# Kernel tuning notes

Hardware: AMD Instinct MI355X
Metric: run time of the kernel (lower is better)

The kernel has to match this reference:

```python
import jax, jax.numpy as jnp
import numpy as np


def _div_tree_level(n_agents, level):
    # Deterministic reproduction of get_division_tree (seeded shuffle), row `level`.
    rng = np.random.RandomState(0)
    perm = rng.permutation(n_agents)
    max_div = int(np.ceil(np.log2(n_agents)))
    levels = np.zeros((max_div + 1, n_agents), dtype=np.int64)
    for ith in range(1, max_div + 1):
        levels[ith] = levels[ith - 1]
        for j in range(n_agents):
            seg = j // (n_agents / 2 ** ith)
            if int(seg) % 2 == 1:
                levels[ith, j] += 2 ** (ith - 1)
    res = levels[:, perm]  # res_levels[:, i] = levels[:, agent2divitreeindex[i]]
    return res[level]


def setup_inputs() -> dict:
    B, A, D, H, NA = 4096, 32, 512, 512, 32
    LEVEL = 3  # current_level after change_div_tree_level(3): 8 distinct experts
    key = jax.random.key(0)
    ks = jax.random.split(key, 4)
    x0 = jax.random.normal(ks[0], (B, A, D), dtype=jnp.float32)
    W_shared = jax.random.normal(ks[1], (D, H), dtype=jnp.float32) * 0.02
    b_shared = jnp.zeros((H,), jnp.float32)
    W1 = jax.random.normal(ks[2], (A, H, H), dtype=jnp.float32) * 0.02
    b1 = jnp.zeros((A, H), jnp.float32)
    W2 = jax.random.normal(ks[3], (A, H, NA), dtype=jnp.float32) * 0.02
    b2 = jnp.zeros((A, NA), jnp.float32)
    route = jnp.asarray(_div_tree_level(A, LEVEL), dtype=jnp.int32)  # [A] expert id per agent
    return dict(x0=x0, W_shared=W_shared, b_shared=b_shared,
                W1=W1, b1=b1, W2=W2, b2=b2, route=route)


def reference(x0, W_shared, b_shared, W1, b1, W2, b2, route):
    # shared trunk: Linear + ReLU over all agents at once
    x1 = jax.nn.relu(x0 @ W_shared + b_shared)          # [B, A, H]
    # static MoE dispatch: gather each agent's expert weights, batched GEMM per agent slot
    Wg1, bg1 = W1[route], b1[route]                     # [A, H, H], [A, H]
    Wg2, bg2 = W2[route], b2[route]                     # [A, H, NA], [A, NA]
    h = jax.nn.relu(jnp.einsum('bah,ahk->bak', x1, Wg1) + bg1)   # [B, A, H]
    x2 = jnp.einsum('bah,ahk->bak', h, Wg2) + bg2       # [B, A, NA]
    return x2
```

## Files before the change

### kernel.cpp

```cpp
#include <hip/hip_runtime.h>
#include <cstdint>
#include <cstddef>

typedef __bf16 bf16x8 __attribute__((ext_vector_type(8)));
typedef float f32x4 __attribute__((ext_vector_type(4)));
typedef unsigned short u16;
typedef u16 u16x4 __attribute__((ext_vector_type(4)));

__device__ __forceinline__ u16 f2bf(float f) {
  union { float f; unsigned u; } v; v.f = f;
  return (u16)((v.u + 0x7FFFu + ((v.u >> 16) & 1u)) >> 16);
}

__device__ __forceinline__ void gl_lds16(const void* g, void* l) {
  __builtin_amdgcn_global_load_lds((__attribute__((address_space(1))) void*)(g),
                                   (__attribute__((address_space(3))) void*)(l), 16, 0, 0);
}

__global__ void transpose_cvt(const float* __restrict__ in, const int* __restrict__ route,
                              u16* __restrict__ out, int K, int N) {
  __shared__ float t[32][33];
  const int a = blockIdx.z;
  const int src = route ? route[a] : a;
  const float* ip = in + (size_t)src * K * N;
  u16* op = out + (size_t)a * K * N;
  const int k0 = blockIdx.x * 32, n0 = blockIdx.y * 32;
  const int tx = threadIdx.x, ty = threadIdx.y;
#pragma unroll
  for (int i = 0; i < 4; ++i)
    t[ty + i * 8][tx] = ip[(size_t)(k0 + ty + i * 8) * N + n0 + tx];
  __syncthreads();
#pragma unroll
  for (int i = 0; i < 4; ++i)
    op[(size_t)(n0 + ty + i * 8) * K + k0 + tx] = f2bf(t[tx][ty + i * 8]);
}

__global__ __launch_bounds__(512)
void fused_mlp(const float* __restrict__ X0, const u16* __restrict__ Wst,
               const float* __restrict__ bsh, const u16* __restrict__ W1t,
               const float* __restrict__ b1, const u16* __restrict__ W2t,
               const float* __restrict__ b2, const int* __restrict__ route,
               float* __restrict__ Out) {
  __shared__ u16 lds[69632];
  u16* Xs = lds;
  u16* Bp0 = lds + 32768;
  u16* Bp1 = lds + 49152;
  u16* Ap0 = lds + 65536;
  u16* Ap1 = lds + 67584;

  const int tid = threadIdx.x;
  const int w = tid >> 6, l = tid & 63;
  const int r = l & 15, q = l >> 4;
  const int a = blockIdx.y;
  const int b0 = blockIdx.x * 64;
  const int rt = route[a];

  int aoff[4], boff[4];
#pragma unroll
  for (int t = 0; t < 4; ++t) {
    aoff[t] = (t * 16 + r) * 32 + ((q ^ ((r >> 1) & 3)) << 3);
    boff[t] = (w * 64 + t * 16 + r) * 32 + ((q ^ ((r >> 1) & 3)) << 3);
  }

  int bdst[4]; int bsrc[4];
#pragma unroll
  for (int c = 0; c < 4; ++c) {
    const int p2 = c * 512 + tid;
    const int n = p2 >> 2, s = p2 & 3;
    bsrc[c] = n * 512 + ((s ^ ((n >> 1) & 3)) << 3);
    bdst[c] = p2 * 8;
  }

  const int arow = tid >> 3, akq = tid & 7;
  const float* gA = X0 + ((size_t)(b0 + arow) * 32 + a) * 512 + akq * 4;
  const int adst = arow * 32 + (((akq >> 1) ^ ((arow >> 1) & 3)) << 3) + (akq & 1) * 4;

  f32x4 acc[4][4];

#pragma unroll
  for (int mt = 0; mt < 4; ++mt)
#pragma unroll
    for (int nt = 0; nt < 4; ++nt) acc[mt][nt] = (f32x4){0.f, 0.f, 0.f, 0.f};

  float4 av = *(const float4*)gA;
#pragma unroll
  for (int c = 0; c < 4; ++c) gl_lds16(Wst + bsrc[c], &Bp0[bdst[c]]);
  {
    const u16x4 d = { f2bf(av.x), f2bf(av.y), f2bf(av.z), f2bf(av.w) };
    *(u16x4*)&Ap0[adst] = d;
  }
  __syncthreads();

  for (int kt = 0; kt < 16; ++kt) {
    const u16* Bc = (kt & 1) ? Bp1 : Bp0;
    const u16* Ac = (kt & 1) ? Ap1 : Ap0;
    u16* Bn = (kt & 1) ? Bp0 : Bp1;
    u16* An = (kt & 1) ? Ap0 : Ap1;
    if (kt < 15) {
      av = *(const float4*)(gA + (kt + 1) * 32);
#pragma unroll
      for (int c = 0; c < 4; ++c)
        gl_lds16(Wst + bsrc[c] + (kt + 1) * 32, &Bn[bdst[c]]);
    }
    bf16x8 af[4], bv[4];
#pragma unroll
    for (int t = 0; t < 4; ++t) af[t] = *(const bf16x8*)&Ac[aoff[t]];
#pragma unroll
    for (int t = 0; t < 4; ++t) bv[t] = *(const bf16x8*)&Bc[boff[t]];
#pragma unroll
    for (int mt = 0; mt < 4; ++mt)
#pragma unroll
      for (int nt = 0; nt < 4; ++nt)
        acc[mt][nt] = __builtin_amdgcn_mfma_f32_16x16x32_bf16(bv[nt], af[mt], acc[mt][nt], 0, 0, 0);
    if (kt < 15) {
      const u16x4 d = { f2bf(av.x), f2bf(av.y), f2bf(av.z), f2bf(av.w) };
      *(u16x4*)&An[adst] = d;
    }
    __syncthreads();
  }
#pragma unroll
  for (int mt = 0; mt < 4; ++mt) {
    const int m = mt * 16 + r;
#pragma unroll
    for (int nt = 0; nt < 4; ++nt) {
      const int col = w * 64 + nt * 16 + q * 4;
      const int gp = (col >> 3) ^ (m & 7);
      const float4 bb = *(const float4*)&bsh[col];
      const f32x4 v = acc[mt][nt];
      const u16x4 d = { f2bf(fmaxf(v.x + bb.x, 0.f)), f2bf(fmaxf(v.y + bb.y, 0.f)),
                        f2bf(fmaxf(v.z + bb.z, 0.f)), f2bf(fmaxf(v.w + bb.w, 0.f)) };
      *(u16x4*)&Xs[m * 512 + gp * 8 + (q & 1) * 4] = d;
    }
  }

  const u16* W1a = W1t + (size_t)a * 262144;
#pragma unroll
  for (int c = 0; c < 4; ++c) gl_lds16(W1a + bsrc[c], &Bp0[bdst[c]]);
  __syncthreads();

#pragma unroll
  for (int mt = 0; mt < 4; ++mt)
#pragma unroll
    for (int nt = 0; nt < 4; ++nt) acc[mt][nt] = (f32x4){0.f, 0.f, 0.f, 0.f};

  for (int kt = 0; kt < 16; ++kt) {
    const u16* Bc = (kt & 1) ? Bp1 : Bp0;
    u16* Bn = (kt & 1) ? Bp0 : Bp1;
    if (kt < 15) {
#pragma unroll
      for (int c = 0; c < 4; ++c)
        gl_lds16(W1a + bsrc[c] + (kt + 1) * 32, &Bn[bdst[c]]);
    }
    bf16x8 af[4], bv[4];
#pragma unroll
    for (int t = 0; t < 4; ++t) {
      const int m = t * 16 + r;
      af[t] = *(const bf16x8*)&Xs[m * 512 + (((kt * 4 + q) ^ (m & 7)) << 3)];
    }
#pragma unroll
    for (int t = 0; t < 4; ++t) bv[t] = *(const bf16x8*)&Bc[boff[t]];
#pragma unroll
    for (int mt = 0; mt < 4; ++mt)
#pragma unroll
      for (int nt = 0; nt < 4; ++nt)
        acc[mt][nt] = __builtin_amdgcn_mfma_f32_16x16x32_bf16(bv[nt], af[mt], acc[mt][nt], 0, 0, 0);
    __syncthreads();
  }

  const u16* W2a = W2t + (size_t)a * 16384;
#pragma unroll
  for (int c = 0; c < 4; ++c) {
    const int p2 = c * 512 + tid;
    const int n = p2 >> 6, gs = p2 & 63;
    gl_lds16(W2a + (size_t)n * 512 + ((gs ^ (n & 7)) << 3), &Bp0[p2 * 8]);
  }
#pragma unroll
  for (int mt = 0; mt < 4; ++mt) {
    const int m = mt * 16 + r;
#pragma unroll
    for (int nt = 0; nt < 4; ++nt) {
      const int col = w * 64 + nt * 16 + q * 4;
      const int gp = (col >> 3) ^ (m & 7);
      const float4 bb = *(const float4*)&b1[(size_t)rt * 512 + col];
      const f32x4 v = acc[mt][nt];
      const u16x4 d = { f2bf(fmaxf(v.x + bb.x, 0.f)), f2bf(fmaxf(v.y + bb.y, 0.f)),
                        f2bf(fmaxf(v.z + bb.z, 0.f)), f2bf(fmaxf(v.w + bb.w, 0.f)) };
      *(u16x4*)&Xs[m * 512 + gp * 8 + (q & 1) * 4] = d;
    }
  }
  __syncthreads();

  {
    const int mt3 = w & 3, nt3 = w >> 2;
    const int m = mt3 * 16 + r;
    const int n = nt3 * 16 + r;
    f32x4 o = (f32x4){0.f, 0.f, 0.f, 0.f};
#pragma unroll
    for (int kt = 0; kt < 16; ++kt) {
      const bf16x8 af = *(const bf16x8*)&Xs[m * 512 + (((kt * 4 + q) ^ (m & 7)) << 3)];
      const bf16x8 bf = *(const bf16x8*)&Bp0[n * 512 + (((kt * 4 + q) ^ (n & 7)) << 3)];
      o = __builtin_amdgcn_mfma_f32_16x16x32_bf16(bf, af, o, 0, 0, 0);
    }
    const int col = nt3 * 16 + q * 4;
    const float4 bb = *(const float4*)&b2[rt * 32 + col];
    const float4 res = { o.x + bb.x, o.y + bb.y, o.z + bb.z, o.w + bb.w };
    *(float4*)&Out[(size_t)(b0 + m) * 1024 + a * 32 + col] = res;
  }
}

extern "C" void kernel_launch(void* const* d_in, const int* in_sizes, int n_in,
                              void* d_out, int out_size, void* d_ws, size_t ws_size,
                              hipStream_t stream) {
  (void)in_sizes; (void)n_in; (void)out_size; (void)ws_size;
  const float* x0  = (const float*)d_in[0];
  const float* Wsh = (const float*)d_in[1];
  const float* bsh = (const float*)d_in[2];
  const float* W1  = (const float*)d_in[3];
  const float* b1  = (const float*)d_in[4];
  const float* W2  = (const float*)d_in[5];
  const float* b2  = (const float*)d_in[6];
  const int* route = (const int*)d_in[7];
  float* out = (float*)d_out;

  char* ws = (char*)d_ws;
  u16* Wst = (u16*)(ws + 0);
  u16* W1t = (u16*)(ws + 524288);
  u16* W2t = (u16*)(ws + 524288 + 16777216);

  transpose_cvt<<<dim3(16, 16, 1),  dim3(32, 8), 0, stream>>>(Wsh, nullptr, Wst, 512, 512);
  transpose_cvt<<<dim3(16, 16, 32), dim3(32, 8), 0, stream>>>(W1, route, W1t, 512, 512);
  transpose_cvt<<<dim3(16, 1, 32),  dim3(32, 8), 0, stream>>>(W2, route, W2t, 512, 32);
  fused_mlp<<<dim3(64, 32), 512, 0, stream>>>(x0, Wst, bsh, W1t, b1, W2t, b2, route, out);
}
```

Before: 614.6 us.

## Split fused MLP into trunk GEMM and per-agent expert GEMM kernels

The single fused kernel is split in two. The first computes the shared trunk GEMM over all rows with 64x512 tiles and writes bf16 activations to workspace in agent-major order. The second streams those activations with direct global-to-LDS loads for the expert GEMMs, reads W2 straight from global memory, and uses 256-thread blocks with two blocks per CU. Double buffering is dropped in favour of single-buffer sync loops. This trades an extra bf16 round trip of the intermediate activations through HBM for smaller LDS use and higher occupancy.

New measurement: 630.7 us. 2.6% more time.

```diff
diff --git a/kernel.cpp b/kernel.cpp
--- a/kernel.cpp
+++ b/kernel.cpp
@@ -6,6 +6,7 @@
 typedef float f32x4 __attribute__((ext_vector_type(4)));
 typedef unsigned short u16;
 typedef u16 u16x4 __attribute__((ext_vector_type(4)));
+typedef u16 u16x8 __attribute__((ext_vector_type(8)));
 
 __device__ __forceinline__ u16 f2bf(float f) {
   union { float f; unsigned u; } v; v.f = f;
@@ -35,18 +36,97 @@
     op[(size_t)(n0 + ty + i * 8) * K + k0 + tx] = f2bf(t[tx][ty + i * 8]);
 }
 
-__global__ __launch_bounds__(512)
-void fused_mlp(const float* __restrict__ X0, const u16* __restrict__ Wst,
-               const float* __restrict__ bsh, const u16* __restrict__ W1t,
-               const float* __restrict__ b1, const u16* __restrict__ W2t,
-               const float* __restrict__ b2, const int* __restrict__ route,
-               float* __restrict__ Out) {
-  __shared__ u16 lds[69632];
-  u16* Xs = lds;
-  u16* Bp0 = lds + 32768;
-  u16* Bp1 = lds + 49152;
-  u16* Ap0 = lds + 65536;
-  u16* Ap1 = lds + 67584;
+__global__ __launch_bounds__(256, 2)
+void gemm1(const float* __restrict__ X0, const u16* __restrict__ Wst,
+           const float* __restrict__ bsh, u16* __restrict__ X1) {
+  __shared__ u16 As[2048];
+  __shared__ u16 Bs[16384];
+  const int tid = threadIdx.x;
+  const int w = tid >> 6, l = tid & 63;
+  const int r = l & 15, q = l >> 4;
+  const int m0 = blockIdx.x * 64;
+
+  const int arow = tid >> 2, akq = tid & 3;
+  const float* gA = X0 + (size_t)(m0 + arow) * 512 + akq * 8;
+  const int adst = arow * 32 + ((akq ^ ((arow >> 1) & 3)) << 3);
+
+  int bsrc[8], bdst[8];
+#pragma unroll
+  for (int c = 0; c < 8; ++c) {
+    const int p = c * 256 + tid;
+    const int n = p >> 2, s = p & 3;
+    bsrc[c] = n * 512 + ((s ^ ((n >> 1) & 3)) << 3);
+    bdst[c] = p * 8;
+  }
+
+  int aoff[4], boff[8];
+#pragma unroll
+  for (int t = 0; t < 4; ++t)
+    aoff[t] = (t * 16 + r) * 32 + ((q ^ ((r >> 1) & 3)) << 3);
+#pragma unroll
+  for (int t = 0; t < 8; ++t)
+    boff[t] = (w * 128 + t * 16 + r) * 32 + ((q ^ ((r >> 1) & 3)) << 3);
+
+  f32x4 acc[4][8];
+#pragma unroll
+  for (int mt = 0; mt < 4; ++mt)
+#pragma unroll
+    for (int nt = 0; nt < 8; ++nt) acc[mt][nt] = (f32x4){0.f, 0.f, 0.f, 0.f};
+
+  float4 a0 = *(const float4*)gA;
+  float4 a1 = *(const float4*)(gA + 4);
+
+  for (int kt = 0; kt < 16; ++kt) {
+    __syncthreads();
+#pragma unroll
+    for (int c = 0; c < 8; ++c) gl_lds16(Wst + bsrc[c] + kt * 32, &Bs[bdst[c]]);
+    {
+      const u16x8 d = { f2bf(a0.x), f2bf(a0.y), f2bf(a0.z), f2bf(a0.w),
+                        f2bf(a1.x), f2bf(a1.y), f2bf(a1.z), f2bf(a1.w) };
+      *(u16x8*)&As[adst] = d;
+    }
+    __syncthreads();
+    if (kt < 15) {
+      a0 = *(const float4*)(gA + (kt + 1) * 32);
+      a1 = *(const float4*)(gA + (kt + 1) * 32 + 4);
+    }
+    bf16x8 af[4], bv[8];
+#pragma unroll
+    for (int t = 0; t < 4; ++t) af[t] = *(const bf16x8*)&As[aoff[t]];
+#pragma unroll
+    for (int t = 0; t < 8; ++t) bv[t] = *(const bf16x8*)&Bs[boff[t]];
+#pragma unroll
+    for (int mt = 0; mt < 4; ++mt)
+#pragma unroll
+      for (int nt = 0; nt < 8; ++nt)
+        acc[mt][nt] = __builtin_amdgcn_mfma_f32_16x16x32_bf16(bv[nt], af[mt], acc[mt][nt], 0, 0, 0);
+  }
+
+#pragma unroll
+  for (int mt = 0; mt < 4; ++mt) {
+    const int m = m0 + mt * 16 + r;
+    u16* orow = X1 + ((size_t)(m & 31) * 4096 + (size_t)(m >> 5)) * 512;
+#pragma unroll
+    for (int nt = 0; nt < 8; ++nt) {
+      const int col = w * 128 + nt * 16 + q * 4;
+      const float4 bb = *(const float4*)&bsh[col];
+      const f32x4 v = acc[mt][nt];
+      const u16x4 d = { f2bf(fmaxf(v.x + bb.x, 0.f)), f2bf(fmaxf(v.y + bb.y, 0.f)),
+                        f2bf(fmaxf(v.z + bb.z, 0.f)), f2bf(fmaxf(v.w + bb.w, 0.f)) };
+      *(u16x4*)&orow[col] = d;
+    }
+  }
+}
+
+__global__ __launch_bounds__(256, 2)
+void gemm23(const u16* __restrict__ X1, const u16* __restrict__ W1t,
+            const float* __restrict__ b1, const u16* __restrict__ W2t,
+            const float* __restrict__ b2, const int* __restrict__ route,
+            float* __restrict__ Out) {
+  __shared__ u16 lds[33280];
+  u16* As = lds;
+  u16* Bs = lds + 2048;
+  u16* Hs = lds;
 
   const int tid = threadIdx.x;
   const int w = tid >> 6, l = tid & 63;
@@ -54,157 +134,90 @@
   const int a = blockIdx.y;
   const int b0 = blockIdx.x * 64;
   const int rt = route[a];
-
-  int aoff[4], boff[4];
-#pragma unroll
-  for (int t = 0; t < 4; ++t) {
+  const u16* X1a = X1 + (size_t)a * 4096 * 512;
+  const u16* W1a = W1t + (size_t)a * 262144;
+  const u16* W2a = W2t + (size_t)a * 16384;
+
+  const int arow = tid >> 2, as_ = tid & 3;
+  const int asrc = (b0 + arow) * 512 + ((as_ ^ ((arow >> 1) & 3)) << 3);
+  const int adst = tid * 8;
+  int bsrc[8], bdst[8];
+#pragma unroll
+  for (int c = 0; c < 8; ++c) {
+    const int p = c * 256 + tid;
+    const int n = p >> 2, s = p & 3;
+    bsrc[c] = n * 512 + ((s ^ ((n >> 1) & 3)) << 3);
+    bdst[c] = p * 8;
+  }
+  int aoff[4], boff[8];
+#pragma unroll
+  for (int t = 0; t < 4; ++t)
     aoff[t] = (t * 16 + r) * 32 + ((q ^ ((r >> 1) & 3)) << 3);
-    boff[t] = (w * 64 + t * 16 + r) * 32 + ((q ^ ((r >> 1) & 3)) << 3);
-  }
-
-  int bdst[4]; int bsrc[4];
-#pragma unroll
-  for (int c = 0; c < 4; ++c) {
-    const int p2 = c * 512 + tid;
-    const int n = p2 >> 2, s = p2 & 3;
-    bsrc[c] = n * 512 + ((s ^ ((n >> 1) & 3)) << 3);
-    bdst[c] = p2 * 8;
-  }
-
-  const int arow = tid >> 3, akq = tid & 7;
-  const float* gA = X0 + ((size_t)(b0 + arow) * 32 + a) * 512 + akq * 4;
-  const int adst = arow * 32 + (((akq >> 1) ^ ((arow >> 1) & 3)) << 3) + (akq & 1) * 4;
-
-  f32x4 acc[4][4];
-
+#pragma unroll
+  for (int t = 0; t < 8; ++t)
+    boff[t] = (w * 128 + t * 16 + r) * 32 + ((q ^ ((r >> 1) & 3)) << 3);
+
+  f32x4 acc[4][8];
 #pragma unroll
   for (int mt = 0; mt < 4; ++mt)
 #pragma unroll
-    for (int nt = 0; nt < 4; ++nt) acc[mt][nt] = (f32x4){0.f, 0.f, 0.f, 0.f};
-
-  float4 av = *(const float4*)gA;
-#pragma unroll
-  for (int c = 0; c < 4; ++c) gl_lds16(Wst + bsrc[c], &Bp0[bdst[c]]);
-  {
-    const u16x4 d = { f2bf(av.x), f2bf(av.y), f2bf(av.z), f2bf(av.w) };
-    *(u16x4*)&Ap0[adst] = d;
+    for (int nt = 0; nt < 8; ++nt) acc[mt][nt] = (f32x4){0.f, 0.f, 0.f, 0.f};
+
+  for (int kt = 0; kt < 16; ++kt) {
+    __syncthreads();
+    gl_lds16(X1a + asrc + kt * 32, &As[adst]);
+#pragma unroll
+    for (int c = 0; c < 8; ++c) gl_lds16(W1a + bsrc[c] + kt * 32, &Bs[bdst[c]]);
+    __syncthreads();
+    bf16x8 af[4], bv[8];
+#pragma unroll
+    for (int t = 0; t < 4; ++t) af[t] = *(const bf16x8*)&As[aoff[t]];
+#pragma unroll
+    for (int t = 0; t < 8; ++t) bv[t] = *(const bf16x8*)&Bs[boff[t]];
+#pragma unroll
+    for (int mt = 0; mt < 4; ++mt)
+#pragma unroll
+      for (int nt = 0; nt < 8; ++nt)
+        acc[mt][nt] = __builtin_amdgcn_mfma_f32_16x16x32_bf16(bv[nt], af[mt], acc[mt][nt], 0, 0, 0);
   }
   __syncthreads();
 
-  for (int kt = 0; kt < 16; ++kt) {
-    const u16* Bc = (kt & 1) ? Bp1 : Bp0;
-    const u16* Ac = (kt & 1) ? Ap1 : Ap0;
-    u16* Bn = (kt & 1) ? Bp0 : Bp1;
-    u16* An = (kt & 1) ? Ap0 : Ap1;
-    if (kt < 15) {
-      av = *(const float4*)(gA + (kt + 1) * 32);
-#pragma unroll
-      for (int c = 0; c < 4; ++c)
-        gl_lds16(Wst + bsrc[c] + (kt + 1) * 32, &Bn[bdst[c]]);
-    }
-    bf16x8 af[4], bv[4];
-#pragma unroll
-    for (int t = 0; t < 4; ++t) af[t] = *(const bf16x8*)&Ac[aoff[t]];
-#pragma unroll
-    for (int t = 0; t < 4; ++t) bv[t] = *(const bf16x8*)&Bc[boff[t]];
-#pragma unroll
-    for (int mt = 0; mt < 4; ++mt)
-#pragma unroll
-      for (int nt = 0; nt < 4; ++nt)
-        acc[mt][nt] = __builtin_amdgcn_mfma_f32_16x16x32_bf16(bv[nt], af[mt], acc[mt][nt], 0, 0, 0);
-    if (kt < 15) {
-      const u16x4 d = { f2bf(av.x), f2bf(av.y), f2bf(av.z), f2bf(av.w) };
-      *(u16x4*)&An[adst] = d;
-    }
-    __syncthreads();
-  }
 #pragma unroll
   for (int mt = 0; mt < 4; ++mt) {
     const int m = mt * 16 + r;
 #pragma unroll
-    for (int nt = 0; nt < 4; ++nt) {
-      const int col = w * 64 + nt * 16 + q * 4;
-      const int gp = (col >> 3) ^ (m & 7);
-      const float4 bb = *(const float4*)&bsh[col];
-      const f32x4 v = acc[mt][nt];
-      const u16x4 d = { f2bf(fmaxf(v.x + bb.x, 0.f)), f2bf(fmaxf(v.y + bb.y, 0.f)),
-                        f2bf(fmaxf(v.z + bb.z, 0.f)), f2bf(fmaxf(v.w + bb.w, 0.f)) };
-      *(u16x4*)&Xs[m * 512 + gp * 8 + (q & 1) * 4] = d;
-    }
-  }
-
-  const u16* W1a = W1t + (size_t)a * 262144;
-#pragma unroll
-  for (int c = 0; c < 4; ++c) gl_lds16(W1a + bsrc[c], &Bp0[bdst[c]]);
-  __syncthreads();
-
-#pragma unroll
-  for (int mt = 0; mt < 4; ++mt)
-#pragma unroll
-    for (int nt = 0; nt < 4; ++nt) acc[mt][nt] = (f32x4){0.f, 0.f, 0.f, 0.f};
-
-  for (int kt = 0; kt < 16; ++kt) {
-    const u16* Bc = (kt & 1) ? Bp1 : Bp0;
-    u16* Bn = (kt & 1) ? Bp0 : Bp1;
-    if (kt < 15) {
-#pragma unroll
-      for (int c = 0; c < 4; ++c)
-        gl_lds16(W1a + bsrc[c] + (kt + 1) * 32, &Bn[bdst[c]]);
-    }
-    bf16x8 af[4], bv[4];
-#pragma unroll
-    for (int t = 0; t < 4; ++t) {
-      const int m = t * 16 + r;
-      af[t] = *(const bf16x8*)&Xs[m * 512 + (((kt * 4 + q) ^ (m & 7)) << 3)];
-    }
-#pragma unroll
-    for (int t = 0; t < 4; ++t) bv[t] = *(const bf16x8*)&Bc[boff[t]];
-#pragma unroll
-    for (int mt = 0; mt < 4; ++mt)
-#pragma unroll
-      for (int nt = 0; nt < 4; ++nt)
-        acc[mt][nt] = __builtin_amdgcn_mfma_f32_16x16x32_bf16(bv[nt], af[mt], acc[mt][nt], 0, 0, 0);
-    __syncthreads();
-  }
-
-  const u16* W2a = W2t + (size_t)a * 16384;
-#pragma unroll
-  for (int c = 0; c < 4; ++c) {
-    const int p2 = c * 512 + tid;
-    const int n = p2 >> 6, gs = p2 & 63;
-    gl_lds16(W2a + (size_t)n * 512 + ((gs ^ (n & 7)) << 3), &Bp0[p2 * 8]);
-  }
-#pragma unroll
-  for (int mt = 0; mt < 4; ++mt) {
-    const int m = mt * 16 + r;
-#pragma unroll
-    for (int nt = 0; nt < 4; ++nt) {
-      const int col = w * 64 + nt * 16 + q * 4;
-      const int gp = (col >> 3) ^ (m & 7);
+    for (int nt = 0; nt < 8; ++nt) {
+      const int col = w * 128 + nt * 16 + q * 4;
       const float4 bb = *(const float4*)&b1[(size_t)rt * 512 + col];
       const f32x4 v = acc[mt][nt];
       const u16x4 d = { f2bf(fmaxf(v.x + bb.x, 0.f)), f2bf(fmaxf(v.y + bb.y, 0.f)),
                         f2bf(fmaxf(v.z + bb.z, 0.f)), f2bf(fmaxf(v.w + bb.w, 0.f)) };
-      *(u16x4*)&Xs[m * 512 + gp * 8 + (q & 1) * 4] = d;
+      *(u16x4*)&Hs[m * 520 + col] = d;
     }
   }
   __syncthreads();
 
   {
-    const int mt3 = w & 3, nt3 = w >> 2;
-    const int m = mt3 * 16 + r;
-    const int n = nt3 * 16 + r;
-    f32x4 o = (f32x4){0.f, 0.f, 0.f, 0.f};
-#pragma unroll
+    const int m = w * 16 + r;
+    f32x4 o[2] = { (f32x4){0.f, 0.f, 0.f, 0.f}, (f32x4){0.f, 0.f, 0.f, 0.f} };
+#pragma unroll 4
     for (int kt = 0; kt < 16; ++kt) {
-      const bf16x8 af = *(const bf16x8*)&Xs[m * 512 + (((kt * 4 + q) ^ (m & 7)) << 3)];
-      const bf16x8 bf = *(const bf16x8*)&Bp0[n * 512 + (((kt * 4 + q) ^ (n & 7)) << 3)];
-      o = __builtin_amdgcn_mfma_f32_16x16x32_bf16(bf, af, o, 0, 0, 0);
-    }
-    const int col = nt3 * 16 + q * 4;
-    const float4 bb = *(const float4*)&b2[rt * 32 + col];
-    const float4 res = { o.x + bb.x, o.y + bb.y, o.z + bb.z, o.w + bb.w };
-    *(float4*)&Out[(size_t)(b0 + m) * 1024 + a * 32 + col] = res;
+      bf16x8 bf[2];
+#pragma unroll
+      for (int nt = 0; nt < 2; ++nt)
+        bf[nt] = *(const bf16x8*)&W2a[(nt * 16 + r) * 512 + kt * 32 + q * 8];
+      const bf16x8 af = *(const bf16x8*)&Hs[m * 520 + kt * 32 + q * 8];
+#pragma unroll
+      for (int nt = 0; nt < 2; ++nt)
+        o[nt] = __builtin_amdgcn_mfma_f32_16x16x32_bf16(bf[nt], af, o[nt], 0, 0, 0);
+    }
+#pragma unroll
+    for (int nt = 0; nt < 2; ++nt) {
+      const int col = nt * 16 + q * 4;
+      const float4 bb = *(const float4*)&b2[rt * 32 + col];
+      const float4 res = { o[nt].x + bb.x, o[nt].y + bb.y, o[nt].z + bb.z, o[nt].w + bb.w };
+      *(float4*)&Out[(size_t)(b0 + m) * 1024 + a * 32 + col] = res;
+    }
   }
 }
 
@@ -226,9 +239,11 @@
   u16* Wst = (u16*)(ws + 0);
   u16* W1t = (u16*)(ws + 524288);
   u16* W2t = (u16*)(ws + 524288 + 16777216);
+  u16* X1  = (u16*)(ws + 18350080);
 
   transpose_cvt<<<dim3(16, 16, 1),  dim3(32, 8), 0, stream>>>(Wsh, nullptr, Wst, 512, 512);
   transpose_cvt<<<dim3(16, 16, 32), dim3(32, 8), 0, stream>>>(W1, route, W1t, 512, 512);
   transpose_cvt<<<dim3(16, 1, 32),  dim3(32, 8), 0, stream>>>(W2, route, W2t, 512, 32);
-  fused_mlp<<<dim3(64, 32), 512, 0, stream>>>(x0, Wst, bsh, W1t, b1, W2t, b2, route, out);
-}
+  gemm1<<<dim3(2048), 256, 0, stream>>>(x0, Wst, bsh, X1);
+  gemm23<<<dim3(64, 32), 256, 0, stream>>>(X1, W1t, b1, W2t, b2, route, out);
+}
```
